# Kernel optimization log

Measured on AMD Instinct MI355X. Metric: run time of the kernel, lower is better.

The kernel has to match this reference:

```python
import jax, jax.numpy as jnp
import numpy as np

B, L, D, E, K = 4, 4096, 2048, 8, 2
ENTROPY_THRESHOLD = 1.0
CAPACITY_FACTOR = 1.25
EPS = 1e-8


def setup_inputs() -> dict:
    key = jax.random.key(0)
    k0, k1, k2 = jax.random.split(key, 3)
    x = jax.random.normal(k0, (B, L, D), jnp.float32)
    gate_W = jax.random.normal(k1, (E, D), jnp.float32) * 0.02
    gate_b = jnp.zeros((E,), jnp.float32)
    expert_W = jax.random.normal(k2, (E, D, D), jnp.float32) * 0.02
    expert_b = jnp.zeros((E, D), jnp.float32)
    return {
        "x": x,
        "gate_W": gate_W,
        "gate_b": gate_b,
        "entropy_weight": jnp.ones((1,), jnp.float32),
        "confidence_weight": jnp.ones((1,), jnp.float32),
        "uncertainty_weight": jnp.ones((1,), jnp.float32),
        "temperature": jnp.ones((1,), jnp.float32),
        "expert_W": expert_W,
        "expert_b": expert_b,
    }


def reference(x, gate_W, gate_b, entropy_weight, confidence_weight,
              uncertainty_weight, temperature, expert_W, expert_b):
    # ---- Entropy-based gating ----
    logits = jnp.einsum('bld,ed->ble', x, gate_W) + gate_b          # (B,L,E)
    base_probs = jax.nn.softmax(logits / temperature[0], axis=-1)
    entropy = -jnp.sum(base_probs * jnp.log(base_probs + EPS), axis=-1)   # (B,L)
    uncertainty = jnp.var(base_probs, axis=-1, ddof=1)              # torch.var unbiased=True
    confidence = 1.0 / (uncertainty + EPS)
    entropy_norm = jax.nn.sigmoid(entropy / ENTROPY_THRESHOLD)
    adaptive = jax.nn.sigmoid(entropy_weight[0] * entropy_norm
                              + confidence_weight[0] * confidence
                              + uncertainty_weight[0] * uncertainty)
    modified = base_probs * (1.0 + adaptive[..., None])
    modified = modified / jnp.sum(modified, axis=-1, keepdims=True)

    # ---- Top-k dispatch weights ----
    topk_vals, topk_idx = jax.lax.top_k(modified, K)                # (B,L,K)
    wnorm = jnp.maximum(jnp.sum(topk_vals, axis=-1, keepdims=True), 1e-9)
    nvals = topk_vals / wnorm
    dispatch = jnp.sum(jax.nn.one_hot(topk_idx, E, dtype=x.dtype) * nvals[..., None], axis=2)  # (B,L,E)

    # ---- Capacity masking via cumsum over sequence ----
    capacity = int(CAPACITY_FACTOR * (B * L / max(1, E)) + 0.9999)
    assign_mask = (dispatch > 0).astype(x.dtype)
    positions = jnp.cumsum(assign_mask, axis=1) - 1.0
    keep = (positions < float(capacity)).astype(x.dtype)
    dispatch = dispatch * keep

    # ---- Dense pooled dispatch / expert / combine ----
    counts = jnp.maximum(jnp.sum(dispatch, axis=1), 1.0)            # (B,E)
    expert_inputs = jnp.einsum('bld,ble->bed', x, dispatch) / counts[..., None]  # (B,E,D)
    expert_outputs = jnp.einsum('bed,efd->bef', expert_inputs, expert_W) + expert_b  # (B,E,D)
    out = jnp.einsum('bed,ble->bld', expert_outputs, dispatch)      # (B,L,D)

    # ---- Aux losses ----
    mean_gate = jnp.mean(base_probs, axis=1)                        # (B,E)
    aux = jnp.var(mean_gate) * E                                    # unbiased=False over all elems
    util = jnp.sum(dispatch, axis=(0, 1)) / (B * L)                 # (E,)
    aux = aux - jnp.var(util, ddof=1) * 0.01                        # diversity loss (unbiased var)
    aux = aux + (jnp.mean(entropy) - ENTROPY_THRESHOLD) ** 2 * 0.01
    return out, aux
```

## Files before the change

kernel.cpp:

```cpp
#include <hip/hip_runtime.h>
#include <cstdint>
#include <cstddef>

#define BB 4
#define LL 4096
#define DD 2048
#define EE 8
#define NTOK (BB*LL)
#define CAP 2560

__global__ __launch_bounds__(256) void k_gate(
    const float* __restrict__ x, const float* __restrict__ gW,
    const float* __restrict__ gb,
    const float* __restrict__ ew_p, const float* __restrict__ cw_p,
    const float* __restrict__ uw_p, const float* __restrict__ temp_p,
    int* __restrict__ tok_idx, float2* __restrict__ tok_w,
    float* __restrict__ probs_part, float* __restrict__ ent_part)
{
    __shared__ float smem[EE * DD];
    const int tid = threadIdx.x;
    #pragma unroll
    for (int i = 0; i < 16; i++) {
        const int idx = tid + i * 256;
        ((float4*)smem)[idx] = ((const float4*)gW)[idx];
    }
    __syncthreads();

    const int wave = tid >> 6, lane = tid & 63;
    const int tok0 = blockIdx.x * 16 + wave * 4;

    float acc[EE][4];
    #pragma unroll
    for (int e = 0; e < EE; e++)
        #pragma unroll
        for (int t = 0; t < 4; t++) acc[e][t] = 0.f;

    #pragma unroll
    for (int j = 0; j < 8; j++) {
        const int fi = lane + j * 64;
        const float4 xv0 = ((const float4*)(x + (size_t)(tok0 + 0) * DD))[fi];
        const float4 xv1 = ((const float4*)(x + (size_t)(tok0 + 1) * DD))[fi];
        const float4 xv2 = ((const float4*)(x + (size_t)(tok0 + 2) * DD))[fi];
        const float4 xv3 = ((const float4*)(x + (size_t)(tok0 + 3) * DD))[fi];
        #pragma unroll
        for (int e = 0; e < EE; e++) {
            const float4 wv = ((const float4*)(smem + e * DD))[fi];
            acc[e][0] += wv.x*xv0.x + wv.y*xv0.y + wv.z*xv0.z + wv.w*xv0.w;
            acc[e][1] += wv.x*xv1.x + wv.y*xv1.y + wv.z*xv1.z + wv.w*xv1.w;
            acc[e][2] += wv.x*xv2.x + wv.y*xv2.y + wv.z*xv2.z + wv.w*xv2.w;
            acc[e][3] += wv.x*xv3.x + wv.y*xv3.y + wv.z*xv3.z + wv.w*xv3.w;
        }
    }
    #pragma unroll
    for (int e = 0; e < EE; e++)
        #pragma unroll
        for (int t = 0; t < 4; t++) {
            float v = acc[e][t];
            v += __shfl_xor(v, 32); v += __shfl_xor(v, 16);
            v += __shfl_xor(v, 8);  v += __shfl_xor(v, 4);
            v += __shfl_xor(v, 2);  v += __shfl_xor(v, 1);
            acc[e][t] = v;
        }
    __syncthreads();

    const float T = temp_p[0];
    #pragma unroll
    for (int t = 0; t < 4; t++) {
        if (lane == t) {
            const int tok = tok0 + t;
            float li[EE];
            #pragma unroll
            for (int e = 0; e < EE; e++) li[e] = (acc[e][t] + gb[e]) / T;
            float mx = li[0];
            #pragma unroll
            for (int e = 1; e < EE; e++) mx = fmaxf(mx, li[e]);
            float p[EE]; float s = 0.f;
            #pragma unroll
            for (int e = 0; e < EE; e++) { p[e] = expf(li[e] - mx); s += p[e]; }
            const float inv = 1.f / s;
            float ent = 0.f, s1 = 0.f;
            #pragma unroll
            for (int e = 0; e < EE; e++) {
                p[e] *= inv;
                ent -= p[e] * logf(p[e] + 1e-8f);
                s1 += p[e];
            }
            const float m = s1 * 0.125f;
            float sv = 0.f;
            #pragma unroll
            for (int e = 0; e < EE; e++) { const float d = p[e] - m; sv += d * d; }
            const float unc  = sv * (1.f / 7.f);
            const float conf = 1.f / (unc + 1e-8f);
            const float enrm = 1.f / (1.f + expf(-ent));
            const float z    = ew_p[0]*enrm + cw_p[0]*conf + uw_p[0]*unc;
            const float ad   = 1.f / (1.f + expf(-z));
            const float fac  = 1.f + ad;
            float md[EE]; float ms = 0.f;
            #pragma unroll
            for (int e = 0; e < EE; e++) { md[e] = p[e] * fac; ms += md[e]; }
            const float minv = 1.f / ms;
            #pragma unroll
            for (int e = 0; e < EE; e++) md[e] *= minv;
            int e0 = 0; float v0 = md[0];
            #pragma unroll
            for (int e = 1; e < EE; e++) { if (md[e] > v0) { v0 = md[e]; e0 = e; } }
            int e1 = 0; float v1 = -1.f;
            #pragma unroll
            for (int e = 0; e < EE; e++) {
                if (e != e0 && md[e] > v1) { v1 = md[e]; e1 = e; }
            }
            const float wn = fmaxf(v0 + v1, 1e-9f);
            tok_idx[tok] = e0 | (e1 << 8);
            tok_w[tok]   = make_float2(v0 / wn, v1 / wn);
            #pragma unroll
            for (int e = 0; e < EE; e++) smem[(wave * 4 + t) * 8 + e] = p[e];
            smem[128 + wave * 4 + t] = ent;
        }
    }
    __syncthreads();
    if (tid < EE) {
        float s = 0.f;
        #pragma unroll
        for (int k = 0; k < 16; k++) s += smem[k * 8 + tid];
        probs_part[blockIdx.x * EE + tid] = s;
    } else if (tid == EE) {
        float s = 0.f;
        #pragma unroll
        for (int k = 0; k < 16; k++) s += smem[128 + k];
        ent_part[blockIdx.x] = s;
    }
}

__global__ __launch_bounds__(256) void k_capacity(
    const int* __restrict__ tok_idx, float2* __restrict__ tok_w,
    float* __restrict__ rawsum)
{
    const int lane = threadIdx.x & 63;
    const int wid  = (blockIdx.x << 2) + (threadIdx.x >> 6);
    const int b = wid >> 3, e = wid & 7;
    int run = 0; float wsum = 0.f;
    for (int c = 0; c < LL / 64; c++) {
        const int t = b * LL + (c << 6) + lane;
        const int idx = tok_idx[t];
        const float2 w = tok_w[t];
        const int e0 = idx & 0xff, e1 = (idx >> 8) & 0xff;
        const bool is0 = (e0 == e), is1 = (e1 == e);
        const float wv = is0 ? w.x : (is1 ? w.y : 0.f);
        const bool assigned = (is0 | is1) && (wv > 0.f);
        const unsigned long long m = __ballot(assigned);
        const int rank = run + __popcll(m & ((1ull << lane) - 1ull));
        const bool keep = assigned && (rank < CAP);
        if (assigned && !keep) {
            if (is0) tok_w[t].x = 0.f; else tok_w[t].y = 0.f;
        }
        float kv = keep ? wv : 0.f;
        kv += __shfl_xor(kv, 32); kv += __shfl_xor(kv, 16);
        kv += __shfl_xor(kv, 8);  kv += __shfl_xor(kv, 4);
        kv += __shfl_xor(kv, 2);  kv += __shfl_xor(kv, 1);
        wsum += kv;
        run  += __popcll(m);
    }
    if (lane == 0) rawsum[wid] = wsum;
}

__global__ __launch_bounds__(256) void k_pool(
    const float* __restrict__ x, const int* __restrict__ tok_idx,
    const float2* __restrict__ tok_w, float* __restrict__ pool_part)
{
    __shared__ float dl[64 * 8];
    const int tid = threadIdx.x;
    const int lc = blockIdx.x, b = blockIdx.y, db = blockIdx.z;
    const int l0 = lc * 64;
    if (tid < 64) {
        const int t = b * LL + l0 + tid;
        const int pk = tok_idx[t];
        const float2 w = tok_w[t];
        #pragma unroll
        for (int e = 0; e < 8; e++) dl[tid * 8 + e] = 0.f;
        dl[tid * 8 + (pk & 0xff)] = w.x;
        dl[tid * 8 + ((pk >> 8) & 0xff)] = w.y;
    }
    __syncthreads();
    const int d0 = db * 1024 + tid * 4;
    float4 acc[8];
    #pragma unroll
    for (int e = 0; e < 8; e++) acc[e] = make_float4(0.f, 0.f, 0.f, 0.f);
    #pragma unroll 4
    for (int l = 0; l < 64; l++) {
        const float4 xv = *((const float4*)(x + ((size_t)(b * LL + l0 + l)) * DD + d0));
        const float4 wA = *((const float4*)(dl + l * 8));
        const float4 wB = *((const float4*)(dl + l * 8 + 4));
        acc[0].x += wA.x*xv.x; acc[0].y += wA.x*xv.y; acc[0].z += wA.x*xv.z; acc[0].w += wA.x*xv.w;
        acc[1].x += wA.y*xv.x; acc[1].y += wA.y*xv.y; acc[1].z += wA.y*xv.z; acc[1].w += wA.y*xv.w;
        acc[2].x += wA.z*xv.x; acc[2].y += wA.z*xv.y; acc[2].z += wA.z*xv.z; acc[2].w += wA.z*xv.w;
        acc[3].x += wA.w*xv.x; acc[3].y += wA.w*xv.y; acc[3].z += wA.w*xv.z; acc[3].w += wA.w*xv.w;
        acc[4].x += wB.x*xv.x; acc[4].y += wB.x*xv.y; acc[4].z += wB.x*xv.z; acc[4].w += wB.x*xv.w;
        acc[5].x += wB.y*xv.x; acc[5].y += wB.y*xv.y; acc[5].z += wB.y*xv.z; acc[5].w += wB.y*xv.w;
        acc[6].x += wB.z*xv.x; acc[6].y += wB.z*xv.y; acc[6].z += wB.z*xv.z; acc[6].w += wB.z*xv.w;
        acc[7].x += wB.w*xv.x; acc[7].y += wB.w*xv.y; acc[7].z += wB.w*xv.z; acc[7].w += wB.w*xv.w;
    }
    #pragma unroll
    for (int e = 0; e < 8; e++)
        *((float4*)(pool_part + (((size_t)lc * BB + b) * EE + e) * DD + d0)) = acc[e];
}

__global__ __launch_bounds__(256) void k_pool_reduce(
    const float* __restrict__ pool_part, const float* __restrict__ rawsum,
    float* __restrict__ ein)
{
    const int d = blockIdx.x * 256 + threadIdx.x;
    const int e = blockIdx.y, b = blockIdx.z;
    float s = 0.f;
    #pragma unroll 8
    for (int lc = 0; lc < 64; lc++)
        s += pool_part[(((size_t)lc * BB + b) * EE + e) * DD + d];
    const float cnt = fmaxf(rawsum[b * EE + e], 1.f);
    ein[((size_t)b * EE + e) * DD + d] = s / cnt;
}

__global__ __launch_bounds__(256) void k_expert(
    const float* __restrict__ ein, const float* __restrict__ eW,
    const float* __restrict__ eb, float* __restrict__ eout)
{
    __shared__ float inl[BB * DD];
    const int tid = threadIdx.x;
    const int e = blockIdx.x >> 9, fb = blockIdx.x & 511;
    #pragma unroll
    for (int i = 0; i < 8; i++) {
        const int idx = tid + i * 256;
        const int bb = idx >> 9, rem = idx & 511;
        ((float4*)inl)[idx] = ((const float4*)ein)[((size_t)bb * EE + e) * 512 + rem];
    }
    __syncthreads();
    const int wave = tid >> 6, lane = tid & 63;
    const int f = fb * 4 + wave;
    const float4* Wrow = (const float4*)(eW + ((size_t)e * DD + f) * DD);
    float a0 = 0.f, a1 = 0.f, a2 = 0.f, a3 = 0.f;
    #pragma unroll
    for (int j = 0; j < 8; j++) {
        const int fi = lane + j * 64;
        const float4 wv = Wrow[fi];
        const float4 i0 = ((const float4*)(inl + 0 * DD))[fi];
        const float4 i1 = ((const float4*)(inl + 1 * DD))[fi];
        const float4 i2 = ((const float4*)(inl + 2 * DD))[fi];
        const float4 i3 = ((const float4*)(inl + 3 * DD))[fi];
        a0 += wv.x*i0.x + wv.y*i0.y + wv.z*i0.z + wv.w*i0.w;
        a1 += wv.x*i1.x + wv.y*i1.y + wv.z*i1.z + wv.w*i1.w;
        a2 += wv.x*i2.x + wv.y*i2.y + wv.z*i2.z + wv.w*i2.w;
        a3 += wv.x*i3.x + wv.y*i3.y + wv.z*i3.z + wv.w*i3.w;
    }
    a0 += __shfl_xor(a0, 32); a0 += __shfl_xor(a0, 16); a0 += __shfl_xor(a0, 8);
    a0 += __shfl_xor(a0, 4);  a0 += __shfl_xor(a0, 2);  a0 += __shfl_xor(a0, 1);
    a1 += __shfl_xor(a1, 32); a1 += __shfl_xor(a1, 16); a1 += __shfl_xor(a1, 8);
    a1 += __shfl_xor(a1, 4);  a1 += __shfl_xor(a1, 2);  a1 += __shfl_xor(a1, 1);
    a2 += __shfl_xor(a2, 32); a2 += __shfl_xor(a2, 16); a2 += __shfl_xor(a2, 8);
    a2 += __shfl_xor(a2, 4);  a2 += __shfl_xor(a2, 2);  a2 += __shfl_xor(a2, 1);
    a3 += __shfl_xor(a3, 32); a3 += __shfl_xor(a3, 16); a3 += __shfl_xor(a3, 8);
    a3 += __shfl_xor(a3, 4);  a3 += __shfl_xor(a3, 2);  a3 += __shfl_xor(a3, 1);
    if (lane == 0) {
        const float bias = eb[e * DD + f];
        eout[((size_t)0 * EE + e) * DD + f] = a0 + bias;
        eout[((size_t)1 * EE + e) * DD + f] = a1 + bias;
        eout[((size_t)2 * EE + e) * DD + f] = a2 + bias;
        eout[((size_t)3 * EE + e) * DD + f] = a3 + bias;
    }
}

__global__ __launch_bounds__(256) void k_combine(
    const int* __restrict__ tok_idx, const float2* __restrict__ tok_w,
    const float* __restrict__ eout, float* __restrict__ out)
{
    const int t = blockIdx.x;
    const int b = t >> 12;
    const int idx = tok_idx[t];
    const float2 w = tok_w[t];
    const int e0 = idx & 0xff, e1 = (idx >> 8) & 0xff;
    const float4* r0 = (const float4*)(eout + ((size_t)b * EE + e0) * DD);
    const float4* r1 = (const float4*)(eout + ((size_t)b * EE + e1) * DD);
    float4* o = (float4*)(out + (size_t)t * DD);
    #pragma unroll
    for (int j = 0; j < 2; j++) {
        const int i = threadIdx.x + j * 256;
        const float4 p0 = r0[i], p1 = r1[i];
        float4 v;
        v.x = w.x * p0.x + w.y * p1.x;
        v.y = w.x * p0.y + w.y * p1.y;
        v.z = w.x * p0.z + w.y * p1.z;
        v.w = w.x * p0.w + w.y * p1.w;
        o[i] = v;
    }
}

__global__ __launch_bounds__(256) void k_aux(
    const float* __restrict__ probs_part, const float* __restrict__ ent_part,
    const float* __restrict__ rawsum, float* __restrict__ aux_out)
{
    __shared__ float sh[256];
    __shared__ float mg[32];
    const int tid = threadIdx.x;
    float es = 0.f;
    for (int i = tid; i < 1024; i += 256) es += ent_part[i];
    sh[tid] = es;
    __syncthreads();
    for (int s = 128; s > 0; s >>= 1) {
        if (tid < s) sh[tid] += sh[tid + s];
        __syncthreads();
    }
    if (tid < 32) {
        const int b = tid >> 3, e = tid & 7;
        float s = 0.f;
        for (int k = 0; k < 256; k++) s += probs_part[((size_t)b * 256 + k) * EE + e];
        mg[tid] = s * (1.f / LL);
    }
    __syncthreads();
    if (tid == 0) {
        const float ment = sh[0] * (1.f / NTOK);
        float msum = 0.f;
        #pragma unroll
        for (int i = 0; i < 32; i++) msum += mg[i];
        const float mm = msum / 32.f;
        float v = 0.f;
        #pragma unroll
        for (int i = 0; i < 32; i++) { const float d = mg[i] - mm; v += d * d; }
        float aux = (v / 32.f) * (float)EE;
        float us = 0.f; float util[8];
        #pragma unroll
        for (int e = 0; e < 8; e++) {
            float u = 0.f;
            #pragma unroll
            for (int b = 0; b < 4; b++) u += rawsum[b * 8 + e];
            u *= (1.f / NTOK);
            util[e] = u; us += u;
        }
        const float um = us / 8.f;
        float uv = 0.f;
        #pragma unroll
        for (int e = 0; e < 8; e++) { const float d = util[e] - um; uv += d * d; }
        uv *= (1.f / 7.f);
        aux -= uv * 0.01f;
        const float de = ment - 1.0f;
        aux += de * de * 0.01f;
        aux_out[0] = aux;
    }
}

extern "C" void kernel_launch(void* const* d_in, const int* in_sizes, int n_in,
                              void* d_out, int out_size, void* d_ws, size_t ws_size,
                              hipStream_t stream)
{
    const float* x  = (const float*)d_in[0];
    const float* gW = (const float*)d_in[1];
    const float* gb = (const float*)d_in[2];
    const float* ew = (const float*)d_in[3];
    const float* cw = (const float*)d_in[4];
    const float* uw = (const float*)d_in[5];
    const float* tp = (const float*)d_in[6];
    const float* eW = (const float*)d_in[7];
    const float* eb = (const float*)d_in[8];
    float* out = (float*)d_out;

    float*  ws         = (float*)d_ws;
    int*    tok_idx    = (int*)ws;
    float2* tok_w      = (float2*)(ws + 16384);
    float*  probs_part = ws + 49152;
    float*  ent_part   = ws + 57344;
    float*  rawsum     = ws + 58368;
    float*  ein        = ws + 58432;
    float*  eout       = ws + 123968;
    float*  pool_part  = out;

    k_gate<<<1024, 256, 0, stream>>>(x, gW, gb, ew, cw, uw, tp,
                                     tok_idx, tok_w, probs_part, ent_part);
    k_capacity<<<8, 256, 0, stream>>>(tok_idx, tok_w, rawsum);
    k_pool<<<dim3(64, 4, 2), 256, 0, stream>>>(x, tok_idx, tok_w, pool_part);
    k_pool_reduce<<<dim3(8, 8, 4), 256, 0, stream>>>(pool_part, rawsum, ein);
    k_expert<<<4096, 256, 0, stream>>>(ein, eW, eb, eout);
    k_combine<<<NTOK, 256, 0, stream>>>(tok_idx, tok_w, eout, out);
    k_aux<<<1, 256, 0, stream>>>(probs_part, ent_part, rawsum,
                                 out + (size_t)NTOK * DD);
}
```

Baseline: 447.1 us.

## Split gate GEMV over D chunks and finalize gating in separate kernel

Splits the gate logit computation into four D-chunks per token group, so each block stages only a 16KB slice of gate weights in LDS instead of 64KB, which raises occupancy and the number of blocks. Partial logits go to a workspace buffer, and a new per-token finalize kernel sums them and runs softmax, entropy, adaptive scaling and top-2. Per-block prob/entropy partials are reduced with a shared-memory tree, and the aux kernel is adjusted to the new count of 64 partial blocks. This adds one kernel launch and a small global round-trip for the partial logits.

```diff
diff --git a/kernel.cpp b/kernel.cpp
--- a/kernel.cpp
+++ b/kernel.cpp
@@ -9,20 +9,18 @@
 #define NTOK (BB*LL)
 #define CAP 2560
 
-__global__ __launch_bounds__(256) void k_gate(
+__global__ __launch_bounds__(256) void k_gate_part(
     const float* __restrict__ x, const float* __restrict__ gW,
-    const float* __restrict__ gb,
-    const float* __restrict__ ew_p, const float* __restrict__ cw_p,
-    const float* __restrict__ uw_p, const float* __restrict__ temp_p,
-    int* __restrict__ tok_idx, float2* __restrict__ tok_w,
-    float* __restrict__ probs_part, float* __restrict__ ent_part)
-{
-    __shared__ float smem[EE * DD];
+    float* __restrict__ gpart)
+{
+    __shared__ float gws[EE * 512];
     const int tid = threadIdx.x;
-    #pragma unroll
-    for (int i = 0; i < 16; i++) {
+    const int kc  = blockIdx.y;
+    #pragma unroll
+    for (int i = 0; i < 4; i++) {
         const int idx = tid + i * 256;
-        ((float4*)smem)[idx] = ((const float4*)gW)[idx];
+        const int e = idx >> 7, c4 = idx & 127;
+        ((float4*)gws)[idx] = ((const float4*)gW)[(size_t)e * 512 + kc * 128 + c4];
     }
     __syncthreads();
 
@@ -36,15 +34,15 @@
         for (int t = 0; t < 4; t++) acc[e][t] = 0.f;
 
     #pragma unroll
-    for (int j = 0; j < 8; j++) {
+    for (int j = 0; j < 2; j++) {
         const int fi = lane + j * 64;
-        const float4 xv0 = ((const float4*)(x + (size_t)(tok0 + 0) * DD))[fi];
-        const float4 xv1 = ((const float4*)(x + (size_t)(tok0 + 1) * DD))[fi];
-        const float4 xv2 = ((const float4*)(x + (size_t)(tok0 + 2) * DD))[fi];
-        const float4 xv3 = ((const float4*)(x + (size_t)(tok0 + 3) * DD))[fi];
+        const float4 xv0 = ((const float4*)x)[(size_t)(tok0 + 0) * 512 + kc * 128 + fi];
+        const float4 xv1 = ((const float4*)x)[(size_t)(tok0 + 1) * 512 + kc * 128 + fi];
+        const float4 xv2 = ((const float4*)x)[(size_t)(tok0 + 2) * 512 + kc * 128 + fi];
+        const float4 xv3 = ((const float4*)x)[(size_t)(tok0 + 3) * 512 + kc * 128 + fi];
         #pragma unroll
         for (int e = 0; e < EE; e++) {
-            const float4 wv = ((const float4*)(smem + e * DD))[fi];
+            const float4 wv = ((const float4*)gws)[e * 128 + fi];
             acc[e][0] += wv.x*xv0.x + wv.y*xv0.y + wv.z*xv0.z + wv.w*xv0.w;
             acc[e][1] += wv.x*xv1.x + wv.y*xv1.y + wv.z*xv1.z + wv.w*xv1.w;
             acc[e][2] += wv.x*xv2.x + wv.y*xv2.y + wv.z*xv2.z + wv.w*xv2.w;
@@ -61,74 +59,100 @@
             v += __shfl_xor(v, 2);  v += __shfl_xor(v, 1);
             acc[e][t] = v;
         }
-    __syncthreads();
-
-    const float T = temp_p[0];
     #pragma unroll
     for (int t = 0; t < 4; t++) {
         if (lane == t) {
-            const int tok = tok0 + t;
-            float li[EE];
+            const size_t base = (size_t)(tok0 + t) * 8 + kc * 2;
+            ((float4*)gpart)[base + 0] = make_float4(acc[0][t], acc[1][t], acc[2][t], acc[3][t]);
+            ((float4*)gpart)[base + 1] = make_float4(acc[4][t], acc[5][t], acc[6][t], acc[7][t]);
+        }
+    }
+}
+
+__global__ __launch_bounds__(256) void k_gate_fin(
+    const float* __restrict__ gpart, const float* __restrict__ gb,
+    const float* __restrict__ ew_p, const float* __restrict__ cw_p,
+    const float* __restrict__ uw_p, const float* __restrict__ temp_p,
+    int* __restrict__ tok_idx, float2* __restrict__ tok_w,
+    float* __restrict__ probs_part, float* __restrict__ ent_part)
+{
+    __shared__ float sh[256 * 9];
+    const int tid = threadIdx.x;
+    const int tok = blockIdx.x * 256 + tid;
+    const float T = temp_p[0];
+
+    float4 r[8];
+    #pragma unroll
+    for (int i = 0; i < 8; i++) r[i] = ((const float4*)gpart)[(size_t)tok * 8 + i];
+
+    float li[EE];
+    li[0] = r[0].x + r[2].x + r[4].x + r[6].x;
+    li[1] = r[0].y + r[2].y + r[4].y + r[6].y;
+    li[2] = r[0].z + r[2].z + r[4].z + r[6].z;
+    li[3] = r[0].w + r[2].w + r[4].w + r[6].w;
+    li[4] = r[1].x + r[3].x + r[5].x + r[7].x;
+    li[5] = r[1].y + r[3].y + r[5].y + r[7].y;
+    li[6] = r[1].z + r[3].z + r[5].z + r[7].z;
+    li[7] = r[1].w + r[3].w + r[5].w + r[7].w;
+    #pragma unroll
+    for (int e = 0; e < EE; e++) li[e] = (li[e] + gb[e]) / T;
+
+    float mx = li[0];
+    #pragma unroll
+    for (int e = 1; e < EE; e++) mx = fmaxf(mx, li[e]);
+    float p[EE]; float s = 0.f;
+    #pragma unroll
+    for (int e = 0; e < EE; e++) { p[e] = expf(li[e] - mx); s += p[e]; }
+    const float inv = 1.f / s;
+    float ent = 0.f, s1 = 0.f;
+    #pragma unroll
+    for (int e = 0; e < EE; e++) {
+        p[e] *= inv;
+        ent -= p[e] * logf(p[e] + 1e-8f);
+        s1 += p[e];
+    }
+    const float m = s1 * 0.125f;
+    float sv = 0.f;
+    #pragma unroll
+    for (int e = 0; e < EE; e++) { const float d = p[e] - m; sv += d * d; }
+    const float unc  = sv * (1.f / 7.f);
+    const float conf = 1.f / (unc + 1e-8f);
+    const float enrm = 1.f / (1.f + expf(-ent));
+    const float z    = ew_p[0]*enrm + cw_p[0]*conf + uw_p[0]*unc;
+    const float ad   = 1.f / (1.f + expf(-z));
+    const float fac  = 1.f + ad;
+    float md[EE]; float ms = 0.f;
+    #pragma unroll
+    for (int e = 0; e < EE; e++) { md[e] = p[e] * fac; ms += md[e]; }
+    const float minv = 1.f / ms;
+    #pragma unroll
+    for (int e = 0; e < EE; e++) md[e] *= minv;
+    int e0 = 0; float v0 = md[0];
+    #pragma unroll
+    for (int e = 1; e < EE; e++) { if (md[e] > v0) { v0 = md[e]; e0 = e; } }
+    int e1 = 0; float v1 = -1.f;
+    #pragma unroll
+    for (int e = 0; e < EE; e++) {
+        if (e != e0 && md[e] > v1) { v1 = md[e]; e1 = e; }
+    }
+    const float wn = fmaxf(v0 + v1, 1e-9f);
+    tok_idx[tok] = e0 | (e1 << 8);
+    tok_w[tok]   = make_float2(v0 / wn, v1 / wn);
+
+    #pragma unroll
+    for (int e = 0; e < EE; e++) sh[tid * 9 + e] = p[e];
+    sh[tid * 9 + 8] = ent;
+    __syncthreads();
+    for (int st = 128; st > 0; st >>= 1) {
+        if (tid < st) {
             #pragma unroll
-            for (int e = 0; e < EE; e++) li[e] = (acc[e][t] + gb[e]) / T;
-            float mx = li[0];
-            #pragma unroll
-            for (int e = 1; e < EE; e++) mx = fmaxf(mx, li[e]);
-            float p[EE]; float s = 0.f;
-            #pragma unroll
-            for (int e = 0; e < EE; e++) { p[e] = expf(li[e] - mx); s += p[e]; }
-            const float inv = 1.f / s;
-            float ent = 0.f, s1 = 0.f;
-            #pragma unroll
-            for (int e = 0; e < EE; e++) {
-                p[e] *= inv;
-                ent -= p[e] * logf(p[e] + 1e-8f);
-                s1 += p[e];
-            }
-            const float m = s1 * 0.125f;
-            float sv = 0.f;
-            #pragma unroll
-            for (int e = 0; e < EE; e++) { const float d = p[e] - m; sv += d * d; }
-            const float unc  = sv * (1.f / 7.f);
-            const float conf = 1.f / (unc + 1e-8f);
-            const float enrm = 1.f / (1.f + expf(-ent));
-            const float z    = ew_p[0]*enrm + cw_p[0]*conf + uw_p[0]*unc;
-            const float ad   = 1.f / (1.f + expf(-z));
-            const float fac  = 1.f + ad;
-            float md[EE]; float ms = 0.f;
-            #pragma unroll
-            for (int e = 0; e < EE; e++) { md[e] = p[e] * fac; ms += md[e]; }
-            const float minv = 1.f / ms;
-            #pragma unroll
-            for (int e = 0; e < EE; e++) md[e] *= minv;
-            int e0 = 0; float v0 = md[0];
-            #pragma unroll
-            for (int e = 1; e < EE; e++) { if (md[e] > v0) { v0 = md[e]; e0 = e; } }
-            int e1 = 0; float v1 = -1.f;
-            #pragma unroll
-            for (int e = 0; e < EE; e++) {
-                if (e != e0 && md[e] > v1) { v1 = md[e]; e1 = e; }
-            }
-            const float wn = fmaxf(v0 + v1, 1e-9f);
-            tok_idx[tok] = e0 | (e1 << 8);
-            tok_w[tok]   = make_float2(v0 / wn, v1 / wn);
-            #pragma unroll
-            for (int e = 0; e < EE; e++) smem[(wave * 4 + t) * 8 + e] = p[e];
-            smem[128 + wave * 4 + t] = ent;
-        }
-    }
-    __syncthreads();
-    if (tid < EE) {
-        float s = 0.f;
-        #pragma unroll
-        for (int k = 0; k < 16; k++) s += smem[k * 8 + tid];
-        probs_part[blockIdx.x * EE + tid] = s;
-    } else if (tid == EE) {
-        float s = 0.f;
-        #pragma unroll
-        for (int k = 0; k < 16; k++) s += smem[128 + k];
-        ent_part[blockIdx.x] = s;
-    }
+            for (int e = 0; e < 9; e++)
+                sh[tid * 9 + e] += sh[(tid + st) * 9 + e];
+        }
+        __syncthreads();
+    }
+    if (tid < EE) probs_part[blockIdx.x * EE + tid] = sh[tid];
+    else if (tid == EE) ent_part[blockIdx.x] = sh[8];
 }
 
 __global__ __launch_bounds__(256) void k_capacity(
@@ -299,7 +323,7 @@
     __shared__ float mg[32];
     const int tid = threadIdx.x;
     float es = 0.f;
-    for (int i = tid; i < 1024; i += 256) es += ent_part[i];
+    if (tid < 64) es = ent_part[tid];
     sh[tid] = es;
     __syncthreads();
     for (int s = 128; s > 0; s >>= 1) {
@@ -309,7 +333,8 @@
     if (tid < 32) {
         const int b = tid >> 3, e = tid & 7;
         float s = 0.f;
-        for (int k = 0; k < 256; k++) s += probs_part[((size_t)b * 256 + k) * EE + e];
+        #pragma unroll
+        for (int k = 0; k < 16; k++) s += probs_part[((size_t)b * 16 + k) * EE + e];
         mg[tid] = s * (1.f / LL);
     }
     __syncthreads();
@@ -367,10 +392,12 @@
     float*  rawsum     = ws + 58368;
     float*  ein        = ws + 58432;
     float*  eout       = ws + 123968;
+    float*  gpart      = ws + 189504;
     float*  pool_part  = out;
 
-    k_gate<<<1024, 256, 0, stream>>>(x, gW, gb, ew, cw, uw, tp,
-                                     tok_idx, tok_w, probs_part, ent_part);
+    k_gate_part<<<dim3(1024, 4), 256, 0, stream>>>(x, gW, gpart);
+    k_gate_fin<<<64, 256, 0, stream>>>(gpart, gb, ew, cw, uw, tp,
+                                       tok_idx, tok_w, probs_part, ent_part);
     k_capacity<<<8, 256, 0, stream>>>(tok_idx, tok_w, rawsum);
     k_pool<<<dim3(64, 4, 2), 256, 0, stream>>>(x, tok_idx, tok_w, pool_part);
     k_pool_reduce<<<dim3(8, 8, 4), 256, 0, stream>>>(pool_part, rawsum, ein);
```

Result: faster. 425.7 us (-4.8%).
